# Kernel tuning notes

Hardware: AMD Instinct MI355X
Metric: run time of the kernel (lower is better)

The kernel has to match this reference:

```python
import jax, jax.numpy as jnp
import numpy as np

NEG = -1e4  # stands in for the -inf diagonal mask (see notes)


def _conv1x1(x, w, b):
    # x: [B,C,H,W], w: [O,C], b: [O]  (1x1 conv == per-pixel matmul)
    return jnp.einsum('bchw,oc->bohw', x, w) + b[None, :, None, None]


def setup_inputs() -> dict:
    key = jax.random.key(0)
    ks = jax.random.split(key, 8)
    B, C, H, W = 32, 64, 128, 128
    q = C // 8
    s = 1.0 / np.sqrt(C).astype(np.float32)
    x = jax.random.normal(ks[0], (B, C, H, W), jnp.float32)
    wq = jax.random.normal(ks[1], (q, C), jnp.float32) * s
    bq = jax.random.normal(ks[2], (q,), jnp.float32) * 0.01
    wk = jax.random.normal(ks[3], (q, C), jnp.float32) * s
    bk = jax.random.normal(ks[4], (q,), jnp.float32) * 0.01
    wv = jax.random.normal(ks[5], (C, C), jnp.float32) * s
    bv = jax.random.normal(ks[6], (C,), jnp.float32) * 0.01
    gamma = jax.random.normal(ks[7], (1,), jnp.float32) * 0.1
    return {'x': x, 'wq': wq, 'bq': bq, 'wk': wk, 'bk': bk,
            'wv': wv, 'bv': bv, 'gamma': gamma}


def reference(x, wq, bq, wk, bk, wv, bv, gamma):
    B, C, H, W = x.shape
    # softplus feature maps on 1x1-conv projections
    Q = jax.nn.softplus(_conv1x1(x, wq, bq))   # [B,q,H,W]
    K = jax.nn.softplus(_conv1x1(x, wk, bk))   # [B,q,H,W]
    V = _conv1x1(x, wv, bv)                    # [B,C,H,W]
    # column (H) energies with masked diagonal, layout [B,H,W,H2]
    diag = jnp.eye(H, dtype=x.dtype)[:, None, :]           # [H,1,H]
    energy_H = jnp.einsum('bqhw,bqkw->bhwk', Q, K) + NEG * diag
    # row (W) energies, layout [B,H,W,W2]
    energy_W = jnp.einsum('bqhw,bqhk->bhwk', Q, K)
    # no softmax in the original forward: energies used as attention weights
    out_H = jnp.einsum('bckw,bhwk->bchw', V, energy_H)
    out_W = jnp.einsum('bchk,bhwk->bchw', V, energy_W)
    return gamma[0] * (out_H + out_W) + x
```

## Files before the change

### kernel.cpp

```cpp
#include <hip/hip_runtime.h>

typedef unsigned short u16;
typedef unsigned int u32;

#define Bn 32
#define Cn 64
#define Hn 128
#define Wn 128
#define QD 8
#define HWn (Hn*Wn)
#define NEGV (-1e4f)

__device__ __forceinline__ float bf2f(u16 u){
  u32 i = ((u32)u) << 16; float f; __builtin_memcpy(&f, &i, 4); return f;
}
__device__ __forceinline__ float bfLO(u32 x){
  u32 i = x << 16; float f; __builtin_memcpy(&f, &i, 4); return f;
}
__device__ __forceinline__ float bfHI(u32 x){
  u32 i = x & 0xFFFF0000u; float f; __builtin_memcpy(&f, &i, 4); return f;
}
__device__ __forceinline__ u16 f2bf(float f){
  u32 i; __builtin_memcpy(&i, &f, 4);
  return (u16)((i + 0x7FFFu + ((i >> 16) & 1u)) >> 16);
}
__device__ __forceinline__ float softplusf(float x){
  return fmaxf(x, 0.0f) + log1pf(expf(-fabsf(x)));
}

__global__ void k_detect(const u32* __restrict__ wq_raw, int* __restrict__ flag){
  __shared__ int cnt;
  if (threadIdx.x == 0) cnt = 0;
  __syncthreads();
  int local = 0;
  for (int i = threadIdx.x; i < 256; i += 64){
    u32 d = wq_raw[i];
    u32 m = (d >> 8) & 0x7Fu;
    if (m >= 0x38u && m <= 0x40u) local++;
  }
  atomicAdd(&cnt, local);
  __syncthreads();
  if (threadIdx.x == 0) flag[0] = (cnt >= 128) ? 1 : 0;
}

__device__ __forceinline__ float rd_any(const void* p, int i, bool bf){
  return bf ? bf2f(((const u16*)p)[i]) : ((const float*)p)[i];
}

__global__ void k_wconv(const void* wq, const void* bq, const void* wk, const void* bk,
                        const void* wv, const void* bv, const void* gamma,
                        const int* __restrict__ flag,
                        float* __restrict__ Wall, float* __restrict__ biasv,
                        float* __restrict__ gammaF){
  bool bf = flag[0] != 0;
  int t = threadIdx.x;
  for (int idx = t; idx < Cn*80; idx += 256){
    int c = idx / 80, j = idx % 80;
    float v;
    if (j < 8)       v = rd_any(wq, j*Cn + c, bf);
    else if (j < 16) v = rd_any(wk, (j-8)*Cn + c, bf);
    else             v = rd_any(wv, (j-16)*Cn + c, bf);
    Wall[idx] = v;
  }
  for (int j = t; j < 80; j += 256){
    float v = (j < 8) ? rd_any(bq, j, bf) : (j < 16) ? rd_any(bk, j-8, bf) : rd_any(bv, j-16, bf);
    biasv[j] = v;
  }
  if (t == 0) gammaF[0] = rd_any(gamma, 0, bf);
}

template<bool BF>
__device__ __forceinline__ void proj_impl(const void* __restrict__ xin,
    const float* __restrict__ Wall, const float* __restrict__ biasv,
    float* __restrict__ Qf, u16* __restrict__ Kb, u16* __restrict__ Vb){
  int b = blockIdx.x >> 6;
  int p = (blockIdx.x & 63)*256 + threadIdx.x;
  float accQ[QD], accK[QD], accV[Cn];
  #pragma unroll
  for (int j=0;j<QD;j++){ accQ[j]=biasv[j]; accK[j]=biasv[QD+j]; }
  #pragma unroll
  for (int j=0;j<Cn;j++) accV[j]=biasv[16+j];
  size_t xoff = (size_t)b*Cn*HWn + p;
  for (int c=0;c<Cn;c++){
    float xv = BF ? bf2f(((const u16*)xin)[xoff + (size_t)c*HWn])
                  : ((const float*)xin)[xoff + (size_t)c*HWn];
    const float* wc = Wall + c*80;
    #pragma unroll
    for (int j=0;j<QD;j++) accQ[j] = fmaf(xv, wc[j], accQ[j]);
    #pragma unroll
    for (int j=0;j<QD;j++) accK[j] = fmaf(xv, wc[QD+j], accK[j]);
    #pragma unroll
    for (int j=0;j<Cn;j++) accV[j] = fmaf(xv, wc[16+j], accV[j]);
  }
  size_t qbase = (size_t)b*QD*HWn + p;
  #pragma unroll
  for (int j=0;j<QD;j++){
    Qf[qbase + (size_t)j*HWn] = softplusf(accQ[j]);
    Kb[qbase + (size_t)j*HWn] = f2bf(softplusf(accK[j]));
  }
  size_t vbase = (size_t)b*Cn*HWn + p;
  #pragma unroll
  for (int j=0;j<Cn;j++) Vb[vbase + (size_t)j*HWn] = f2bf(accV[j]);
}

__global__ __launch_bounds__(256) void k_proj(const void* __restrict__ xin,
    const int* __restrict__ flag, const float* __restrict__ Wall,
    const float* __restrict__ biasv, float* __restrict__ Qf,
    u16* __restrict__ Kb, u16* __restrict__ Vb){
  if (flag[0]) proj_impl<true >(xin, Wall, biasv, Qf, Kb, Vb);
  else         proj_impl<false>(xin, Wall, biasv, Qf, Kb, Vb);
}

__global__ __launch_bounds__(256, 2) void k_msum(const u16* __restrict__ Vb,
    const u16* __restrict__ Kb, float* __restrict__ Mcol, float* __restrict__ Mrow){
  __shared__ u16 Kl[8*16*128];
  __shared__ u16 Vl[4*16*128];
  int b  = blockIdx.x >> 4;
  int ct = blockIdx.x & 15;
  int t  = threadIdx.x;
  float macc[16];
  #pragma unroll
  for (int i=0;i<16;i++) macc[i] = 0.f;
  const u32* kg = (const u32*)(Kb + (size_t)b*QD*HWn);
  const u32* vg = (const u32*)(Vb + ((size_t)b*Cn + ct*4)*HWn);

  for (int ht = 0; ht < Hn/16; ++ht){
    int h0 = ht*16;
    #pragma unroll
    for (int r=0;r<32;r++){
      int f = r*256 + t;
      int q = f >> 10, h = (f >> 6) & 15, w2 = f & 63;
      u32 kv = kg[(size_t)q*(HWn/2) + (size_t)(h0+h)*(Wn/2) + w2];
      int wi = (w2*2) ^ (h<<2);
      *(u32*)&Kl[(q*16+h)*128 + wi] = kv;
    }
    #pragma unroll
    for (int r=0;r<16;r++){
      int f = r*256 + t;
      int c = f >> 10, h = (f >> 6) & 15, w2 = f & 63;
      u32 vv = vg[(size_t)c*(HWn/2) + (size_t)(h0+h)*(Wn/2) + w2];
      int wi = (w2*2) ^ (h<<2);
      *(u32*)&Vl[(c*16+h)*128 + wi] = vv;
    }
    __syncthreads();
    #pragma unroll
    for (int r=0;r<2;r++){
      int idx = r*256 + t;
      int c = idx >> 7, q = (idx >> 4) & 7, h = idx & 15;
      const u16* kr = &Kl[(q*16+h)*128];
      const u16* vr = &Vl[(c*16+h)*128];
      int hs = h << 2;
      float acc = 0.f;
      #pragma unroll 8
      for (int w4=0; w4<32; ++w4){
        int wi = (w4<<2) ^ hs;
        u32 k0 = *(const u32*)&kr[wi];
        u32 k1 = *(const u32*)&kr[wi+2];
        u32 v0 = *(const u32*)&vr[wi];
        u32 v1 = *(const u32*)&vr[wi+2];
        acc = fmaf(bfLO(v0), bfLO(k0), acc);
        acc = fmaf(bfHI(v0), bfHI(k0), acc);
        acc = fmaf(bfLO(v1), bfLO(k1), acc);
        acc = fmaf(bfHI(v1), bfHI(k1), acc);
      }
      Mrow[(((size_t)b*Cn + ct*4 + c)*QD + q)*Hn + h0 + h] = acc;
    }
    #pragma unroll
    for (int r=0;r<4;r++){
      int idx = r*256 + t;
      int c = idx >> 8, q = (idx >> 5) & 7, w4 = idx & 31;
      float a0 = macc[r*4], a1 = macc[r*4+1], a2 = macc[r*4+2], a3 = macc[r*4+3];
      #pragma unroll 4
      for (int h=0; h<16; ++h){
        int wi = ((w4 ^ h) << 2);
        const u16* kr = &Kl[(q*16+h)*128];
        const u16* vr = &Vl[(c*16+h)*128];
        u32 k0 = *(const u32*)&kr[wi];
        u32 k1 = *(const u32*)&kr[wi+2];
        u32 v0 = *(const u32*)&vr[wi];
        u32 v1 = *(const u32*)&vr[wi+2];
        a0 = fmaf(bfLO(v0), bfLO(k0), a0);
        a1 = fmaf(bfHI(v0), bfHI(k0), a1);
        a2 = fmaf(bfLO(v1), bfLO(k1), a2);
        a3 = fmaf(bfHI(v1), bfHI(k1), a3);
      }
      macc[r*4] = a0; macc[r*4+1] = a1; macc[r*4+2] = a2; macc[r*4+3] = a3;
    }
    __syncthreads();
  }
  #pragma unroll
  for (int r=0;r<4;r++){
    int idx = r*256 + t;
    int c = idx >> 8, q = (idx >> 5) & 7, w4 = idx & 31;
    size_t o = (((size_t)b*Cn + ct*4 + c)*QD + q)*Wn + w4*4;
    float4 v; v.x = macc[r*4]; v.y = macc[r*4+1]; v.z = macc[r*4+2]; v.w = macc[r*4+3];
    *(float4*)&Mcol[o] = v;
  }
}

template<bool BF>
__device__ __forceinline__ void final_impl(const void* __restrict__ xin,
    const float* __restrict__ Qf, const u16* __restrict__ Vb,
    const float* __restrict__ Mcol, const float* __restrict__ Mrow,
    const float* __restrict__ gammaF, void* __restrict__ outp, float* mr){
  int b = blockIdx.x >> 4;
  int ht = blockIdx.x & 15;
  int w = threadIdx.x & 127;
  int s = threadIdx.x >> 7;
  int h0 = ht*8;
  float gma = gammaF[0];
  for (int idx = threadIdx.x; idx < Cn*8*QD; idx += 256){
    int c = idx >> 6; int rem = idx & 63; int q = rem >> 3; int hl = rem & 7;
    mr[(c*8 + hl)*QD + q] = Mrow[(((size_t)b*Cn + c)*QD + q)*Hn + h0 + hl];
  }
  __syncthreads();
  float Qr[4][QD];
  #pragma unroll
  for (int i=0;i<4;i++){
    int h = h0 + s*4 + i;
    #pragma unroll
    for (int q=0;q<QD;q++)
      Qr[i][q] = Qf[(((size_t)b*QD + q)*Hn + h)*Wn + w];
  }
  for (int c=0;c<Cn;c++){
    float Mc[QD];
    #pragma unroll
    for (int q=0;q<QD;q++)
      Mc[q] = Mcol[(((size_t)b*Cn + c)*QD + q)*Wn + w];
    size_t base = ((size_t)b*Cn + c)*HWn + (size_t)h0*Wn + w;
    #pragma unroll
    for (int i=0;i<4;i++){
      int hl = s*4 + i;
      size_t off = base + (size_t)hl*Wn;
      float v = bf2f(Vb[off]);
      float acc = NEGV * v;
      #pragma unroll
      for (int q=0;q<QD;q++)
        acc = fmaf(Qr[i][q], Mc[q] + mr[(c*8 + hl)*QD + q], acc);
      float xv = BF ? bf2f(((const u16*)xin)[off]) : ((const float*)xin)[off];
      float res = fmaf(gma, acc, xv);
      if (BF) ((u16*)outp)[off] = f2bf(res);
      else    ((float*)outp)[off] = res;
    }
  }
}

__global__ __launch_bounds__(256) void k_final(const void* __restrict__ xin,
    const int* __restrict__ flag, const float* __restrict__ Qf,
    const u16* __restrict__ Vb, const float* __restrict__ Mcol,
    const float* __restrict__ Mrow, const float* __restrict__ gammaF,
    void* __restrict__ outp){
  __shared__ float mr[Cn*8*QD];
  if (flag[0]) final_impl<true >(xin, Qf, Vb, Mcol, Mrow, gammaF, outp, mr);
  else         final_impl<false>(xin, Qf, Vb, Mcol, Mrow, gammaF, outp, mr);
}

extern "C" void kernel_launch(void* const* d_in, const int* in_sizes, int n_in,
                              void* d_out, int out_size, void* d_ws, size_t ws_size,
                              hipStream_t stream){
  char* ws = (char*)d_ws;
  float* Qf     = (float*)(ws);
  u16*   Kb     = (u16*)  (ws + 16777216);
  float* Mcol   = (float*)(ws + 25165824);
  float* Mrow   = (float*)(ws + 33554432);
  float* Wall   = (float*)(ws + 41943040);
  float* biasv  = (float*)(ws + 41963520);
  float* gammaF = (float*)(ws + 41963840);
  int*   flag   = (int*)  (ws + 41963844);
  u16*   Vb     = (u16*)  (ws + 41964032);

  k_detect<<<1, 64, 0, stream>>>((const u32*)d_in[1], flag);
  k_wconv<<<1, 256, 0, stream>>>(d_in[1], d_in[2], d_in[3], d_in[4],
                                 d_in[5], d_in[6], d_in[7], flag,
                                 Wall, biasv, gammaF);
  k_proj<<<Bn*(HWn/256), 256, 0, stream>>>(d_in[0], flag, Wall, biasv, Qf, Kb, Vb);
  k_msum<<<Bn*16, 256, 0, stream>>>(Vb, Kb, Mcol, Mrow);
  k_final<<<Bn*16, 256, 0, stream>>>(d_in[0], flag, Qf, Vb, Mcol, Mrow, gammaF, d_out);
}
```

Measured before the change: 483.7 us.

## Restructure projection with LDS-staged bf16 input, two pixels per thread, bf16 Q

New measurement: 643.4 us. +33.0%, slower.

```diff
diff --git a/kernel.cpp b/kernel.cpp
--- a/kernel.cpp
+++ b/kernel.cpp
@@ -24,36 +24,33 @@
   u32 i; __builtin_memcpy(&i, &f, 4);
   return (u16)((i + 0x7FFFu + ((i >> 16) & 1u)) >> 16);
 }
+__device__ __forceinline__ u32 pack2bf(float lo, float hi){
+  return (u32)f2bf(lo) | ((u32)f2bf(hi) << 16);
+}
 __device__ __forceinline__ float softplusf(float x){
   return fmaxf(x, 0.0f) + log1pf(expf(-fabsf(x)));
 }
-
-__global__ void k_detect(const u32* __restrict__ wq_raw, int* __restrict__ flag){
-  __shared__ int cnt;
-  if (threadIdx.x == 0) cnt = 0;
-  __syncthreads();
-  int local = 0;
-  for (int i = threadIdx.x; i < 256; i += 64){
-    u32 d = wq_raw[i];
-    u32 m = (d >> 8) & 0x7Fu;
-    if (m >= 0x38u && m <= 0x40u) local++;
-  }
-  atomicAdd(&cnt, local);
-  __syncthreads();
-  if (threadIdx.x == 0) flag[0] = (cnt >= 128) ? 1 : 0;
-}
-
 __device__ __forceinline__ float rd_any(const void* p, int i, bool bf){
   return bf ? bf2f(((const u16*)p)[i]) : ((const float*)p)[i];
 }
 
-__global__ void k_wconv(const void* wq, const void* bq, const void* wk, const void* bk,
+__global__ void k_setup(const void* wq, const void* bq, const void* wk, const void* bk,
                         const void* wv, const void* bv, const void* gamma,
-                        const int* __restrict__ flag,
+                        int* __restrict__ flag,
                         float* __restrict__ Wall, float* __restrict__ biasv,
                         float* __restrict__ gammaF){
-  bool bf = flag[0] != 0;
+  __shared__ int cnt;
   int t = threadIdx.x;
+  if (t == 0) cnt = 0;
+  __syncthreads();
+  {
+    u32 d = ((const u32*)wq)[t];
+    u32 m = (d >> 8) & 0x7Fu;
+    if (m >= 0x38u && m <= 0x40u) atomicAdd(&cnt, 1);
+  }
+  __syncthreads();
+  bool bf = (cnt >= 128);
+  if (t == 0) flag[0] = bf ? 1 : 0;
   for (int idx = t; idx < Cn*80; idx += 256){
     int c = idx / 80, j = idx % 80;
     float v;
@@ -69,46 +66,103 @@
   if (t == 0) gammaF[0] = rd_any(gamma, 0, bf);
 }
 
-template<bool BF>
-__device__ __forceinline__ void proj_impl(const void* __restrict__ xin,
-    const float* __restrict__ Wall, const float* __restrict__ biasv,
-    float* __restrict__ Qf, u16* __restrict__ Kb, u16* __restrict__ Vb){
-  int b = blockIdx.x >> 6;
-  int p = (blockIdx.x & 63)*256 + threadIdx.x;
-  float accQ[QD], accK[QD], accV[Cn];
-  #pragma unroll
-  for (int j=0;j<QD;j++){ accQ[j]=biasv[j]; accK[j]=biasv[QD+j]; }
-  #pragma unroll
-  for (int j=0;j<Cn;j++) accV[j]=biasv[16+j];
-  size_t xoff = (size_t)b*Cn*HWn + p;
-  for (int c=0;c<Cn;c++){
-    float xv = BF ? bf2f(((const u16*)xin)[xoff + (size_t)c*HWn])
-                  : ((const float*)xin)[xoff + (size_t)c*HWn];
-    const float* wc = Wall + c*80;
-    #pragma unroll
-    for (int j=0;j<QD;j++) accQ[j] = fmaf(xv, wc[j], accQ[j]);
-    #pragma unroll
-    for (int j=0;j<QD;j++) accK[j] = fmaf(xv, wc[QD+j], accK[j]);
-    #pragma unroll
-    for (int j=0;j<Cn;j++) accV[j] = fmaf(xv, wc[16+j], accV[j]);
-  }
-  size_t qbase = (size_t)b*QD*HWn + p;
-  #pragma unroll
-  for (int j=0;j<QD;j++){
-    Qf[qbase + (size_t)j*HWn] = softplusf(accQ[j]);
-    Kb[qbase + (size_t)j*HWn] = f2bf(softplusf(accK[j]));
-  }
-  size_t vbase = (size_t)b*Cn*HWn + p;
-  #pragma unroll
-  for (int j=0;j<Cn;j++) Vb[vbase + (size_t)j*HWn] = f2bf(accV[j]);
-}
-
-__global__ __launch_bounds__(256) void k_proj(const void* __restrict__ xin,
+__global__ __launch_bounds__(256, 2) void k_proj(const void* __restrict__ xin,
     const int* __restrict__ flag, const float* __restrict__ Wall,
-    const float* __restrict__ biasv, float* __restrict__ Qf,
+    const float* __restrict__ biasv, u16* __restrict__ Qb,
     u16* __restrict__ Kb, u16* __restrict__ Vb){
-  if (flag[0]) proj_impl<true >(xin, Wall, biasv, Qf, Kb, Vb);
-  else         proj_impl<false>(xin, Wall, biasv, Qf, Kb, Vb);
+  __shared__ u16 xl[Cn*512];
+  int t = threadIdx.x;
+  int b = blockIdx.x >> 5;
+  int p0 = (blockIdx.x & 31) * 512;
+
+  if (flag[0]){
+    const u32* xg = (const u32*)((const u16*)xin + (size_t)b*Cn*HWn + p0);
+    u32* xls = (u32*)xl;
+    #pragma unroll
+    for (int r=0;r<16;r++){
+      int f = r*256 + t;
+      int c = f >> 6, qd = f & 63;
+      *(uint4*)&xls[c*256 + qd*4] = *(const uint4*)&xg[(size_t)c*(HWn/2) + qd*4];
+    }
+    __syncthreads();
+
+    {
+      float aq[QD][2], ak[QD][2];
+      #pragma unroll
+      for (int j=0;j<QD;j++){
+        aq[j][0]=biasv[j];    aq[j][1]=biasv[j];
+        ak[j][0]=biasv[QD+j]; ak[j][1]=biasv[QD+j];
+      }
+      #pragma unroll 2
+      for (int c=0;c<Cn;c++){
+        u32 xv = ((u32*)xl)[c*256 + t];
+        float x0 = bfLO(xv), x1 = bfHI(xv);
+        const float* wc = Wall + c*80;
+        #pragma unroll
+        for (int j=0;j<QD;j++){
+          float wj = wc[j], wk8 = wc[QD+j];
+          aq[j][0] = fmaf(x0, wj, aq[j][0]);  aq[j][1] = fmaf(x1, wj, aq[j][1]);
+          ak[j][0] = fmaf(x0, wk8, ak[j][0]); ak[j][1] = fmaf(x1, wk8, ak[j][1]);
+        }
+      }
+      #pragma unroll
+      for (int j=0;j<QD;j++){
+        size_t o = ((size_t)(b*QD + j)*HWn + p0)/2 + t;
+        ((u32*)Qb)[o] = pack2bf(softplusf(aq[j][0]), softplusf(aq[j][1]));
+        ((u32*)Kb)[o] = pack2bf(softplusf(ak[j][0]), softplusf(ak[j][1]));
+      }
+    }
+    for (int g=0; g<2; ++g){
+      float av[32][2];
+      #pragma unroll
+      for (int j=0;j<32;j++){ av[j][0]=biasv[16+g*32+j]; av[j][1]=av[j][0]; }
+      #pragma unroll 2
+      for (int c=0;c<Cn;c++){
+        u32 xv = ((u32*)xl)[c*256 + t];
+        float x0 = bfLO(xv), x1 = bfHI(xv);
+        const float* wc = Wall + c*80 + 16 + g*32;
+        #pragma unroll
+        for (int j=0;j<32;j++){
+          float wj = wc[j];
+          av[j][0] = fmaf(x0, wj, av[j][0]);  av[j][1] = fmaf(x1, wj, av[j][1]);
+        }
+      }
+      #pragma unroll
+      for (int j=0;j<32;j++){
+        size_t o = ((size_t)(b*Cn + g*32 + j)*HWn + p0)/2 + t;
+        ((u32*)Vb)[o] = pack2bf(av[j][0], av[j][1]);
+      }
+    }
+  } else {
+    for (int sub=0; sub<2; ++sub){
+      int p = p0 + sub*256 + t;
+      float accQ[QD], accK[QD], accV[Cn];
+      #pragma unroll
+      for (int j=0;j<QD;j++){ accQ[j]=biasv[j]; accK[j]=biasv[QD+j]; }
+      #pragma unroll
+      for (int j=0;j<Cn;j++) accV[j]=biasv[16+j];
+      size_t xoff = (size_t)b*Cn*HWn + p;
+      for (int c=0;c<Cn;c++){
+        float xv = ((const float*)xin)[xoff + (size_t)c*HWn];
+        const float* wc = Wall + c*80;
+        #pragma unroll
+        for (int j=0;j<QD;j++) accQ[j] = fmaf(xv, wc[j], accQ[j]);
+        #pragma unroll
+        for (int j=0;j<QD;j++) accK[j] = fmaf(xv, wc[QD+j], accK[j]);
+        #pragma unroll
+        for (int j=0;j<Cn;j++) accV[j] = fmaf(xv, wc[16+j], accV[j]);
+      }
+      size_t qbase = (size_t)b*QD*HWn + p;
+      #pragma unroll
+      for (int j=0;j<QD;j++){
+        Qb[qbase + (size_t)j*HWn] = f2bf(softplusf(accQ[j]));
+        Kb[qbase + (size_t)j*HWn] = f2bf(softplusf(accK[j]));
+      }
+      size_t vbase = (size_t)b*Cn*HWn + p;
+      #pragma unroll
+      for (int j=0;j<Cn;j++) Vb[vbase + (size_t)j*HWn] = f2bf(accV[j]);
+    }
+  }
 }
 
 __global__ __launch_bounds__(256, 2) void k_msum(const u16* __restrict__ Vb,
@@ -200,7 +254,7 @@
 
 template<bool BF>
 __device__ __forceinline__ void final_impl(const void* __restrict__ xin,
-    const float* __restrict__ Qf, const u16* __restrict__ Vb,
+    const u16* __restrict__ Qb, const u16* __restrict__ Vb,
     const float* __restrict__ Mcol, const float* __restrict__ Mrow,
     const float* __restrict__ gammaF, void* __restrict__ outp, float* mr){
   int b = blockIdx.x >> 4;
@@ -220,7 +274,7 @@
     int h = h0 + s*4 + i;
     #pragma unroll
     for (int q=0;q<QD;q++)
-      Qr[i][q] = Qf[(((size_t)b*QD + q)*Hn + h)*Wn + w];
+      Qr[i][q] = bf2f(Qb[(((size_t)b*QD + q)*Hn + h)*Wn + w]);
   }
   for (int c=0;c<Cn;c++){
     float Mc[QD];
@@ -246,34 +300,33 @@
 }
 
 __global__ __launch_bounds__(256) void k_final(const void* __restrict__ xin,
-    const int* __restrict__ flag, const float* __restrict__ Qf,
+    const int* __restrict__ flag, const u16* __restrict__ Qb,
     const u16* __restrict__ Vb, const float* __restrict__ Mcol,
     const float* __restrict__ Mrow, const float* __restrict__ gammaF,
     void* __restrict__ outp){
   __shared__ float mr[Cn*8*QD];
-  if (flag[0]) final_impl<true >(xin, Qf, Vb, Mcol, Mrow, gammaF, outp, mr);
-  else         final_impl<false>(xin, Qf, Vb, Mcol, Mrow, gammaF, outp, mr);
+  if (flag[0]) final_impl<true >(xin, Qb, Vb, Mcol, Mrow, gammaF, outp, mr);
+  else         final_impl<false>(xin, Qb, Vb, Mcol, Mrow, gammaF, outp, mr);
 }
 
 extern "C" void kernel_launch(void* const* d_in, const int* in_sizes, int n_in,
                               void* d_out, int out_size, void* d_ws, size_t ws_size,
                               hipStream_t stream){
   char* ws = (char*)d_ws;
-  float* Qf     = (float*)(ws);
-  u16*   Kb     = (u16*)  (ws + 16777216);
-  float* Mcol   = (float*)(ws + 25165824);
-  float* Mrow   = (float*)(ws + 33554432);
-  float* Wall   = (float*)(ws + 41943040);
-  float* biasv  = (float*)(ws + 41963520);
-  float* gammaF = (float*)(ws + 41963840);
-  int*   flag   = (int*)  (ws + 41963844);
-  u16*   Vb     = (u16*)  (ws + 41964032);
-
-  k_detect<<<1, 64, 0, stream>>>((const u32*)d_in[1], flag);
-  k_wconv<<<1, 256, 0, stream>>>(d_in[1], d_in[2], d_in[3], d_in[4],
+  u16*   Qb     = (u16*)  (ws);
+  u16*   Kb     = (u16*)  (ws + 8388608);
+  float* Mcol   = (float*)(ws + 16777216);
+  float* Mrow   = (float*)(ws + 25165824);
+  float* Wall   = (float*)(ws + 33554432);
+  float* biasv  = (float*)(ws + 33574912);
+  float* gammaF = (float*)(ws + 33575232);
+  int*   flag   = (int*)  (ws + 33575236);
+  u16*   Vb     = (u16*)  (ws + 33575424);
+
+  k_setup<<<1, 256, 0, stream>>>(d_in[1], d_in[2], d_in[3], d_in[4],
                                  d_in[5], d_in[6], d_in[7], flag,
                                  Wall, biasv, gammaF);
-  k_proj<<<Bn*(HWn/256), 256, 0, stream>>>(d_in[0], flag, Wall, biasv, Qf, Kb, Vb);
+  k_proj<<<Bn*(HWn/512), 256, 0, stream>>>(d_in[0], flag, Wall, biasv, Qb, Kb, Vb);
   k_msum<<<Bn*16, 256, 0, stream>>>(Vb, Kb, Mcol, Mrow);
-  k_final<<<Bn*16, 256, 0, stream>>>(d_in[0], flag, Qf, Vb, Mcol, Mrow, gammaF, d_out);
-}
+  k_final<<<Bn*16, 256, 0, stream>>>(d_in[0], flag, Qb, Vb, Mcol, Mrow, gammaF, d_out);
+}
```
